# Kernel optimization log

Measured on AMD Instinct MI355X. Metric: run time of the kernel, lower is better.

The kernel has to match this reference:

```python
import jax, jax.numpy as jnp
import numpy as np

DIAG_MASK = 1e20  # value added on the diagonal to exclude self as negative


def setup_inputs() -> dict:
    key = jax.random.key(0)
    k1, k2, k3 = jax.random.split(key, 3)
    B, D_in, D_out = 4096, 1024, 1024
    anchor_x = jax.random.normal(k1, (B, D_in), dtype=jnp.float32)
    pos_x = jax.random.normal(k2, (B, D_in), dtype=jnp.float32)
    W = jax.random.normal(k3, (D_in, D_out), dtype=jnp.float32) * (1.0 / np.sqrt(D_in))
    b = jnp.zeros((D_out,), dtype=jnp.float32)
    return {"anchor_x": anchor_x, "pos_x": pos_x, "W": W, "b": b}


def reference(anchor_x, pos_x, W, b):
    # Encoder: simple dense projection (stand-in for the wrapped BERT encoder).
    anchor = anchor_x @ W + b          # [B, D]
    pos = pos_x @ W + b                # [B, D]

    # Pairwise squared distances dist[i,j] = ||anchor_i - pos_j||^2,
    # computed via the GEMM identity |a|^2 + |p|^2 - 2 a.p (same math as the
    # original broadcasted (a_i - p_j)^2 reduce_sum, far less memory traffic).
    a2 = jnp.sum(anchor * anchor, axis=-1, keepdims=True)       # [B, 1]
    p2 = jnp.sum(pos * pos, axis=-1, keepdims=True).T           # [1, B]
    dist = a2 + p2 - 2.0 * (anchor @ pos.T)                     # [B, B]

    B = dist.shape[0]
    mask_dist = dist + jnp.eye(B, dtype=dist.dtype) * DIAG_MASK  # mask diagonal
    indices = jnp.argmin(mask_dist, axis=-1)                     # [B] hard negatives
    neg = pos[indices]                                           # gather [B, D]

    return jnp.concatenate([anchor, pos, neg], axis=-1)          # [B, 3D]
```

## Files before the change

### kernel.cpp

```cpp
#include <hip/hip_runtime.h>


typedef short s8v __attribute__((ext_vector_type(8)));
typedef float f4v __attribute__((ext_vector_type(4)));
typedef unsigned short u16;

#define B  4096
#define D  1024
#define OLD 3072
#define OLD16 6144
#define LDK 68

__device__ __forceinline__ u16 f2bf(float f) {
  union { float f; unsigned u; } v; v.f = f;
  unsigned r = v.u + 0x7FFFu + ((v.u >> 16) & 1u);
  return (u16)(r >> 16);
}
__device__ __forceinline__ float bf2f(u16 s) {
  union { unsigned u; float f; } v; v.u = ((unsigned)s) << 16;
  return v.f;
}

__device__ __forceinline__ void gld16(const void* g, void* l) {
  __builtin_amdgcn_global_load_lds(
      (const __attribute__((address_space(1))) unsigned int*)g,
      (__attribute__((address_space(3))) unsigned int*)l, 16, 0, 0);
}

struct Top2 { float v1, v2; int j1, j2; };
__device__ __forceinline__ void t2_insert(Top2& t, float v, int j) {
  if (v < t.v1 || (v == t.v1 && j < t.j1)) {
    t.v2 = t.v1; t.j2 = t.j1; t.v1 = v; t.j1 = j;
  } else if (v < t.v2 || (v == t.v2 && j < t.j2)) {
    t.v2 = v; t.j2 = j;
  }
}
struct Top4 { float v[4]; int j[4]; };
__device__ __forceinline__ void t4_insert(Top4& t, float v, int j) {
  if (v < t.v[3] || (v == t.v[3] && j < t.j[3])) {
    int p = 3;
#pragma unroll
    for (int s = 0; s < 3; ++s) {
      if (p > 0 && (v < t.v[p - 1] || (v == t.v[p - 1] && j < t.j[p - 1]))) {
        t.v[p] = t.v[p - 1]; t.j[p] = t.j[p - 1]; --p;
      }
    }
    t.v[p] = v; t.j[p] = j;
  }
}

__global__ void splitT_W(const float* __restrict__ W, u16* __restrict__ WtQ) {
  __shared__ float tile[32][33];
  const int bx = blockIdx.x * 32, by = blockIdx.y * 32;
  const int tx = threadIdx.x, ty = threadIdx.y;
  for (int dy = 0; dy < 32; dy += 8)
    tile[ty + dy][tx] = W[(size_t)(by + ty + dy) * D + bx + tx];
  __syncthreads();
  for (int dy = 0; dy < 32; dy += 8) {
    const float v = tile[tx][ty + dy];
    const u16 h = f2bf(v);
    const size_t o = (size_t)(bx + ty + dy) * 2048 + by + tx;
    WtQ[o] = h;
    WtQ[o + 1024] = f2bf(v - bf2f(h));
  }
}

__global__ __launch_bounds__(256) void splitX2(
    const float* __restrict__ A, const float* __restrict__ P,
    u16* __restrict__ O16, u16* __restrict__ posXq) {
  const int r = blockIdx.x, t = threadIdx.x;
  const bool isPos = r >= B;
  const int row = isPos ? r - B : r;
  const float4 v = *(const float4*)&(isPos ? P : A)[(size_t)row * D + t * 4];
  const float vv[4] = {v.x, v.y, v.z, v.w};
  ushort4 hi, mi;
  u16* hp = &hi.x; u16* mp = &mi.x;
#pragma unroll
  for (int i = 0; i < 4; ++i) {
    hp[i] = f2bf(vv[i]);
    mp[i] = f2bf(vv[i] - bf2f(hp[i]));
  }
  if (isPos) {
    *(ushort4*)&posXq[(size_t)row * 2048 + t * 4] = hi;
    *(ushort4*)&posXq[(size_t)row * 2048 + 1024 + t * 4] = mi;
  } else {
    *(ushort4*)&O16[(size_t)row * OLD16 + 4096 + t * 4] = hi;
    *(ushort4*)&O16[(size_t)row * OLD16 + 5120 + t * 4] = mi;
  }
}

__global__ __launch_bounds__(256) void enc_mfma(
    float* out, const u16* __restrict__ posXq, const u16* __restrict__ WtQ,
    const float* __restrict__ bias, u16* __restrict__ Aq, u16* __restrict__ Pq) {
  __shared__ __align__(16) u16 lAh[128 * 32], lAm[128 * 32];
  __shared__ __align__(16) u16 lBh[128 * 32], lBm[128 * 32];
  const u16* O16 = (const u16*)out;
  const int tid = threadIdx.x, lane = tid & 63, wave = tid >> 6;
  const int waveM = wave >> 1, waveN = wave & 1;
  const int row16 = lane & 15, quad = lane >> 4;
  const bool isPos = blockIdx.y >= 32;
  const int Mbase = (blockIdx.y & 31) * 128;
  const int Nbase = blockIdx.x * 128;
  f4v acc[4][4] = {};

  for (int kk = 0; kk < D; kk += 32) {
    __syncthreads();
#pragma unroll
    for (int i = 0; i < 2; ++i) {
      const int c = i * 256 + wave * 64 + lane;
      const int row = c >> 2, col8 = (c & 3) * 8;
      const int lo = (i * 256 + wave * 64) * 8;
      if (isPos) {
        gld16(&posXq[(size_t)(Mbase + row) * 2048 + kk + col8], &lAh[lo]);
        gld16(&posXq[(size_t)(Mbase + row) * 2048 + 1024 + kk + col8], &lAm[lo]);
      } else {
        gld16(&O16[(size_t)(Mbase + row) * OLD16 + 4096 + kk + col8], &lAh[lo]);
        gld16(&O16[(size_t)(Mbase + row) * OLD16 + 5120 + kk + col8], &lAm[lo]);
      }
      gld16(&WtQ[(size_t)(Nbase + row) * 2048 + kk + col8], &lBh[lo]);
      gld16(&WtQ[(size_t)(Nbase + row) * 2048 + 1024 + kk + col8], &lBm[lo]);
    }
    __syncthreads();
    s8v ah[4], am[4], bh[4], bm[4];
#pragma unroll
    for (int mi = 0; mi < 4; ++mi) {
      const int ro = (waveM * 64 + mi * 16 + row16) * 32 + quad * 8;
      ah[mi] = *(const s8v*)&lAh[ro];
      am[mi] = *(const s8v*)&lAm[ro];
    }
#pragma unroll
    for (int ni = 0; ni < 4; ++ni) {
      const int ro = (waveN * 64 + ni * 16 + row16) * 32 + quad * 8;
      bh[ni] = *(const s8v*)&lBh[ro];
      bm[ni] = *(const s8v*)&lBm[ro];
    }
#pragma unroll
    for (int mi = 0; mi < 4; ++mi)
#pragma unroll
      for (int ni = 0; ni < 4; ++ni) {
        f4v a = acc[mi][ni];
        a = __builtin_amdgcn_mfma_f32_16x16x32_bf16(ah[mi], bh[ni], a, 0, 0, 0);
        a = __builtin_amdgcn_mfma_f32_16x16x32_bf16(ah[mi], bm[ni], a, 0, 0, 0);
        a = __builtin_amdgcn_mfma_f32_16x16x32_bf16(am[mi], bh[ni], a, 0, 0, 0);
        acc[mi][ni] = a;
      }
  }
  const int outOff = isPos ? 1024 : 0;
  u16* Q = isPos ? Pq : Aq;
#pragma unroll
  for (int ni = 0; ni < 4; ++ni) {
    const int col = Nbase + waveN * 64 + ni * 16 + row16;
    const float bv = bias[col];
#pragma unroll
    for (int mi = 0; mi < 4; ++mi) {
      const int rbase = Mbase + waveM * 64 + mi * 16 + quad * 4;
#pragma unroll
      for (int r = 0; r < 4; ++r) {
        const size_t row = rbase + r;
        const float v = acc[mi][ni][r] + bv;
        out[row * OLD + outOff + col] = v;
        const u16 h = f2bf(v);
        Q[row * 2048 + col] = h;
        Q[row * 2048 + 1024 + col] = f2bf(v - bf2f(h));
      }
    }
  }
}

__global__ __launch_bounds__(256) void pnorm(float* __restrict__ o) {
  const int row = blockIdx.x, t = threadIdx.x;
  const float4 v = *(const float4*)&o[(size_t)row * OLD + D + t * 4];
  float s = v.x * v.x + v.y * v.y + v.z * v.z + v.w * v.w;
#pragma unroll
  for (int off = 32; off; off >>= 1) s += __shfl_down(s, off, 64);
  __shared__ float wsum[4];
  if ((t & 63) == 0) wsum[t >> 6] = s;
  __syncthreads();
  if (t == 0) o[(size_t)row * OLD + 2048] = wsum[0] + wsum[1] + wsum[2] + wsum[3];
}

__global__ __launch_bounds__(256) void dist_mfma(
    const u16* __restrict__ Aq, const u16* __restrict__ Pq, float* __restrict__ o) {
  __shared__ __align__(16) u16 lAh[128 * 32], lAm[128 * 32];
  __shared__ __align__(16) u16 lBh[128 * 32];
  __shared__ float sv1[128][2], sv2[128][2];
  __shared__ int sj1[128][2], sj2[128][2];
  const int tid = threadIdx.x, lane = tid & 63, wave = tid >> 6;
  const int waveM = wave >> 1, waveN = wave & 1;
  const int row16 = lane & 15, quad = lane >> 4;
  const int Mbase = blockIdx.y * 128;
  const int Nbase = blockIdx.x * 128;
  f4v acc[4][4] = {};

  for (int kk = 0; kk < D; kk += 32) {
    __syncthreads();
#pragma unroll
    for (int i = 0; i < 2; ++i) {
      const int c = i * 256 + wave * 64 + lane;
      const int row = c >> 2, col8 = (c & 3) * 8;
      const int lo = (i * 256 + wave * 64) * 8;
      gld16(&Aq[(size_t)(Mbase + row) * 2048 + kk + col8], &lAh[lo]);
      gld16(&Aq[(size_t)(Mbase + row) * 2048 + 1024 + kk + col8], &lAm[lo]);
      gld16(&Pq[(size_t)(Nbase + row) * 2048 + kk + col8], &lBh[lo]);
    }
    __syncthreads();
    s8v ah[4], am[4], bh[4];
#pragma unroll
    for (int i = 0; i < 4; ++i) {
      const int aro = (waveM * 64 + i * 16 + row16) * 32 + quad * 8;
      const int bro = (waveN * 64 + i * 16 + row16) * 32 + quad * 8;
      ah[i] = *(const s8v*)&lAh[aro];
      am[i] = *(const s8v*)&lAm[aro];
      bh[i] = *(const s8v*)&lBh[bro];
    }
#pragma unroll
    for (int mi = 0; mi < 4; ++mi)
#pragma unroll
      for (int ni = 0; ni < 4; ++ni) {
        f4v a = acc[mi][ni];
        a = __builtin_amdgcn_mfma_f32_16x16x32_bf16(ah[mi], bh[ni], a, 0, 0, 0);
        a = __builtin_amdgcn_mfma_f32_16x16x32_bf16(am[mi], bh[ni], a, 0, 0, 0);
        acc[mi][ni] = a;
      }
  }

  float p2c[4];
#pragma unroll
  for (int ni = 0; ni < 4; ++ni)
    p2c[ni] = o[(size_t)(Nbase + waveN * 64 + ni * 16 + row16) * OLD + 2048];
#pragma unroll
  for (int mi = 0; mi < 4; ++mi)
#pragma unroll
    for (int r = 0; r < 4; ++r) {
      const int rg = Mbase + waveM * 64 + mi * 16 + quad * 4 + r;
      Top2 tp; tp.v1 = 3.0e38f; tp.v2 = 3.0e38f; tp.j1 = 0; tp.j2 = 1;
#pragma unroll
      for (int ni = 0; ni < 4; ++ni) {
        const int cg = Nbase + waveN * 64 + ni * 16 + row16;
        if (cg != rg) t2_insert(tp, p2c[ni] - 2.0f * acc[mi][ni][r], cg);
      }
#pragma unroll
      for (int m = 1; m < 16; m <<= 1) {
        const float ov1 = __shfl_xor(tp.v1, m, 64);
        const int oj1 = __shfl_xor(tp.j1, m, 64);
        const float ov2 = __shfl_xor(tp.v2, m, 64);
        const int oj2 = __shfl_xor(tp.j2, m, 64);
        t2_insert(tp, ov1, oj1);
        t2_insert(tp, ov2, oj2);
      }
      if (row16 == 0) {
        const int rl = waveM * 64 + mi * 16 + quad * 4 + r;
        sv1[rl][waveN] = tp.v1; sj1[rl][waveN] = tp.j1;
        sv2[rl][waveN] = tp.v2; sj2[rl][waveN] = tp.j2;
      }
    }
  __syncthreads();
  if (tid < 128) {
    Top2 tp; tp.v1 = sv1[tid][0]; tp.j1 = sj1[tid][0];
    tp.v2 = sv2[tid][0]; tp.j2 = sj2[tid][0];
    t2_insert(tp, sv1[tid][1], sj1[tid][1]);
    t2_insert(tp, sv2[tid][1], sj2[tid][1]);
    ((float4*)&o[(size_t)(Mbase + tid) * OLD + 2056])[blockIdx.x] =
        make_float4(tp.v1, __int_as_float(tp.j1), tp.v2, __int_as_float(tp.j2));
  }
}

__global__ __launch_bounds__(256) void argmin_refine(float* __restrict__ o) {
  const int i = blockIdx.x, t = threadIdx.x;
  __shared__ int gj[4];
  if (t < 64) {
    Top4 tp;
#pragma unroll
    for (int c = 0; c < 4; ++c) { tp.v[c] = 3.0e38f; tp.j[c] = 0; }
    if (t < 32) {
      const float4 p = ((const float4*)&o[(size_t)i * OLD + 2056])[t];
      t4_insert(tp, p.x, __float_as_int(p.y));
      t4_insert(tp, p.z, __float_as_int(p.w));
    }
#pragma unroll
    for (int m = 1; m < 32; m <<= 1) {
#pragma unroll
      for (int c = 0; c < 4; ++c) {
        const float ov = __shfl_xor(tp.v[c], m, 64);
        const int oj = __shfl_xor(tp.j[c], m, 64);
        t4_insert(tp, ov, oj);
      }
    }
    if (t == 0) {
#pragma unroll
      for (int c = 0; c < 4; ++c)
        gj[c] = (tp.j[c] < 0) ? 0 : (tp.j[c] > B - 1 ? B - 1 : tp.j[c]);
    }
  }
  __syncthreads();
  int jj[4];
#pragma unroll
  for (int c = 0; c < 4; ++c) jj[c] = gj[c];
  const float4 a4 = *(const float4*)&o[(size_t)i * OLD + t * 4];
  float s[4], n[4];
#pragma unroll
  for (int c = 0; c < 4; ++c) {
    const float4 q = *(const float4*)&o[(size_t)jj[c] * OLD + D + t * 4];
    s[c] = a4.x * q.x + a4.y * q.y + a4.z * q.z + a4.w * q.w;
    n[c] = q.x * q.x + q.y * q.y + q.z * q.z + q.w * q.w;
  }
#pragma unroll
  for (int off = 32; off; off >>= 1)
#pragma unroll
    for (int c = 0; c < 4; ++c) {
      s[c] += __shfl_down(s[c], off, 64);
      n[c] += __shfl_down(n[c], off, 64);
    }
  __shared__ float wsum[4][8];
  __shared__ int sjf;
  if ((t & 63) == 0)
#pragma unroll
    for (int c = 0; c < 4; ++c) {
      wsum[t >> 6][c] = s[c];
      wsum[t >> 6][4 + c] = n[c];
    }
  __syncthreads();
  if (t == 0) {
    float bd = 3.4e38f; int bj = 0x7fffffff;
#pragma unroll
    for (int c = 0; c < 4; ++c) {
      const float S = wsum[0][c] + wsum[1][c] + wsum[2][c] + wsum[3][c];
      const float N = wsum[0][4 + c] + wsum[1][4 + c] + wsum[2][4 + c] + wsum[3][4 + c];
      const float d = N - 2.0f * S;
      const int j = jj[c];
      if (d < bd || (d == bd && j < bj)) { bd = d; bj = j; }
    }
    sjf = bj;
  }
  __syncthreads();
  const int j = sjf;
  ((float4*)&o[(size_t)i * OLD + 2048])[t] = ((const float4*)&o[(size_t)j * OLD + D])[t];
}

__global__ __launch_bounds__(256) void enc_gemm(
    const float* __restrict__ X, const float* __restrict__ W,
    const float* __restrict__ bia, float* __restrict__ out, int outOff) {
  __shared__ float lA[32][LDK];
  __shared__ float lW[32][LDK];
  const int tid = threadIdx.x;
  const int Mbase = blockIdx.y * 64;
  const int Nbase = blockIdx.x * 64;
  const int ty = tid >> 4, tx = tid & 15;
  float acc[4][4] = {};
  for (int k0 = 0; k0 < D; k0 += 32) {
    __syncthreads();
#pragma unroll
    for (int h = 0; h < 2; ++h) {
      const int ch = tid + h * 256;
      const int r = ch >> 3, c4 = (ch & 7) * 4;
      const float4 a4 = *(const float4*)&X[(size_t)(Mbase + r) * D + k0 + c4];
      lA[c4 + 0][r] = a4.x; lA[c4 + 1][r] = a4.y;
      lA[c4 + 2][r] = a4.z; lA[c4 + 3][r] = a4.w;
      const int kr = ch >> 4, nc = (ch & 15) * 4;
      *(float4*)&lW[kr][nc] = *(const float4*)&W[(size_t)(k0 + kr) * D + Nbase + nc];
    }
    __syncthreads();
#pragma unroll
    for (int kk = 0; kk < 32; ++kk) {
      const float4 av = *(const float4*)&lA[kk][ty * 4];
      const float4 wv = *(const float4*)&lW[kk][tx * 4];
      acc[0][0] += av.x * wv.x; acc[0][1] += av.x * wv.y; acc[0][2] += av.x * wv.z; acc[0][3] += av.x * wv.w;
      acc[1][0] += av.y * wv.x; acc[1][1] += av.y * wv.y; acc[1][2] += av.y * wv.z; acc[1][3] += av.y * wv.w;
      acc[2][0] += av.z * wv.x; acc[2][1] += av.z * wv.y; acc[2][2] += av.z * wv.z; acc[2][3] += av.z * wv.w;
      acc[3][0] += av.w * wv.x; acc[3][1] += av.w * wv.y; acc[3][2] += av.w * wv.z; acc[3][3] += av.w * wv.w;
    }
  }
  const float4 b4 = *(const float4*)&bia[Nbase + tx * 4];
#pragma unroll
  for (int i = 0; i < 4; ++i) {
    const int row = Mbase + ty * 4 + i;
    float4 ov;
    ov.x = acc[i][0] + b4.x; ov.y = acc[i][1] + b4.y;
    ov.z = acc[i][2] + b4.z; ov.w = acc[i][3] + b4.w;
    *(float4*)&out[(size_t)row * OLD + outOff + Nbase + tx * 4] = ov;
  }
}

__global__ __launch_bounds__(256) void dist_argmin_f32(float* __restrict__ o) {
  __shared__ float lA[32][LDK];
  __shared__ float lB[32][LDK];
  const int tid = threadIdx.x;
  const int Mbase = blockIdx.y * 64, Nbase = blockIdx.x * 64;
  const int ty = tid >> 4, tx = tid & 15;
  float acc[4][4] = {};
  for (int k0 = 0; k0 < D; k0 += 32) {
    __syncthreads();
#pragma unroll
    for (int h = 0; h < 2; ++h) {
      const int ch = tid + h * 256;
      const int r = ch >> 3, c4 = (ch & 7) * 4;
      const float4 a4 = *(const float4*)&o[(size_t)(Mbase + r) * OLD + k0 + c4];
      const float4 b4 = *(const float4*)&o[(size_t)(Nbase + r) * OLD + D + k0 + c4];
      lA[c4 + 0][r] = a4.x; lA[c4 + 1][r] = a4.y;
      lA[c4 + 2][r] = a4.z; lA[c4 + 3][r] = a4.w;
      lB[c4 + 0][r] = b4.x; lB[c4 + 1][r] = b4.y;
      lB[c4 + 2][r] = b4.z; lB[c4 + 3][r] = b4.w;
    }
    __syncthreads();
#pragma unroll
    for (int kk = 0; kk < 32; ++kk) {
      const float4 av = *(const float4*)&lA[kk][ty * 4];
      const float4 bv = *(const float4*)&lB[kk][tx * 4];
      acc[0][0] += av.x * bv.x; acc[0][1] += av.x * bv.y; acc[0][2] += av.x * bv.z; acc[0][3] += av.x * bv.w;
      acc[1][0] += av.y * bv.x; acc[1][1] += av.y * bv.y; acc[1][2] += av.y * bv.z; acc[1][3] += av.y * bv.w;
      acc[2][0] += av.z * bv.x; acc[2][1] += av.z * bv.y; acc[2][2] += av.z * bv.z; acc[2][3] += av.z * bv.w;
      acc[3][0] += av.w * bv.x; acc[3][1] += av.w * bv.y; acc[3][2] += av.w * bv.z; acc[3][3] += av.w * bv.w;
    }
  }
  float colp2[4];
#pragma unroll
  for (int j = 0; j < 4; ++j)
    colp2[j] = o[(size_t)(Nbase + tx * 4 + j) * OLD + 2048];
#pragma unroll
  for (int i = 0; i < 4; ++i) {
    const int rg = Mbase + ty * 4 + i;
    float bv = 3.0e38f; int bj = 0;
#pragma unroll
    for (int j = 0; j < 4; ++j) {
      const int cg = Nbase + tx * 4 + j;
      const float d = colp2[j] - 2.0f * acc[i][j];
      if (cg != rg && d < bv) { bv = d; bj = cg; }
    }
#pragma unroll
    for (int m = 1; m < 16; m <<= 1) {
      const float ov = __shfl_xor(bv, m, 64);
      const int oj = __shfl_xor(bj, m, 64);
      if (ov < bv || (ov == bv && oj < bj)) { bv = ov; bj = oj; }
    }
    if (tx == 0)
      ((float2*)&o[(size_t)rg * OLD + 2056])[blockIdx.x] =
          make_float2(bv, __int_as_float(bj));
  }
}

__global__ __launch_bounds__(256) void argmin_final_f2(float* __restrict__ o, int nblk) {
  const int i = blockIdx.x, t = threadIdx.x;
  __shared__ int sj;
  if (t < 64) {
    float v = 3.4e38f; int j = 0x7fffffff;
    if (t < nblk) {
      const float2 p = ((const float2*)&o[(size_t)i * OLD + 2056])[t];
      v = p.x; j = __float_as_int(p.y);
    }
#pragma unroll
    for (int m = 32; m; m >>= 1) {
      const float ov = __shfl_xor(v, m, 64);
      const int oj = __shfl_xor(j, m, 64);
      if (ov < v || (ov == v && oj < j)) { v = ov; j = oj; }
    }
    if (t == 0) sj = (j < 0) ? 0 : (j > B - 1 ? B - 1 : j);
  }
  __syncthreads();
  const int j = sj;
  ((float4*)&o[(size_t)i * OLD + 2048])[t] = ((const float4*)&o[(size_t)j * OLD + D])[t];
}

extern "C" void kernel_launch(void* const* d_in, const int* in_sizes, int n_in,
                              void* d_out, int out_size, void* d_ws, size_t ws_size,
                              hipStream_t stream) {
  const float* anchor_x = (const float*)d_in[0];
  const float* pos_x    = (const float*)d_in[1];
  const float* W        = (const float*)d_in[2];
  const float* b        = (const float*)d_in[3];
  float* out = (float*)d_out;
  char* ws = (char*)d_ws;
  const size_t MB = 1024 * 1024;

  if (ws_size >= 52 * MB) {
    u16* Aq     = (u16*)(ws);
    u16* Pq     = (u16*)(ws + 16 * MB);
    u16* WtQ    = (u16*)(ws + 32 * MB);
    u16* posXq  = (u16*)(ws + 36 * MB);
    splitT_W<<<dim3(32, 32), dim3(32, 8), 0, stream>>>(W, WtQ);
    splitX2<<<2 * B, 256, 0, stream>>>(anchor_x, pos_x, (u16*)out, posXq);
    enc_mfma<<<dim3(8, 64), 256, 0, stream>>>(out, posXq, WtQ, b, Aq, Pq);
    pnorm<<<B, 256, 0, stream>>>(out);
    dist_mfma<<<dim3(32, 32), 256, 0, stream>>>(Aq, Pq, out);
    argmin_refine<<<B, 256, 0, stream>>>(out);
  } else {
    enc_gemm<<<dim3(16, 64), 256, 0, stream>>>(anchor_x, W, b, out, 0);
    enc_gemm<<<dim3(16, 64), 256, 0, stream>>>(pos_x,    W, b, out, 1024);
    pnorm<<<B, 256, 0, stream>>>(out);
    dist_argmin_f32<<<dim3(64, 64), 256, 0, stream>>>(out);
    argmin_final_f2<<<B, 256, 0, stream>>>(out, 64);
  }
}
```

Measured before the change: 318.6 us.

## Use single fp16 MFMA for distance GEMM with double-buffered swizzled LDS

The distance GEMM now stores anchor and positive embeddings as one fp16 value each instead of a bf16 hi/lo pair. This halves that GEMM's operand traffic and MFMA count, since two bf16 MFMAs per tile become one fp16 MFMA. Both the encoder and distance GEMMs also gain double-buffered LDS staging with an XOR swizzle on the K-chunk slot, so the next tile loads while the current one computes and LDS bank conflicts are reduced. The cost is lower precision in the dot products that feed the coarse argmin, which a later refine pass must absorb, and the doubled LDS footprint may lower occupancy.

```diff
diff --git a/kernel.cpp b/kernel.cpp
--- a/kernel.cpp
+++ b/kernel.cpp
@@ -2,6 +2,7 @@
 
 
 typedef short s8v __attribute__((ext_vector_type(8)));
+typedef _Float16 h8v __attribute__((ext_vector_type(8)));
 typedef float f4v __attribute__((ext_vector_type(4)));
 typedef unsigned short u16;
 
@@ -91,9 +92,10 @@
 
 __global__ __launch_bounds__(256) void enc_mfma(
     float* out, const u16* __restrict__ posXq, const u16* __restrict__ WtQ,
-    const float* __restrict__ bias, u16* __restrict__ Aq, u16* __restrict__ Pq) {
-  __shared__ __align__(16) u16 lAh[128 * 32], lAm[128 * 32];
-  __shared__ __align__(16) u16 lBh[128 * 32], lBm[128 * 32];
+    const float* __restrict__ bias, _Float16* __restrict__ Aq,
+    _Float16* __restrict__ Pq) {
+  __shared__ __align__(16) u16 lAh[2][128 * 32], lAm[2][128 * 32];
+  __shared__ __align__(16) u16 lBh[2][128 * 32], lBm[2][128 * 32];
   const u16* O16 = (const u16*)out;
   const int tid = threadIdx.x, lane = tid & 63, wave = tid >> 6;
   const int waveM = wave >> 1, waveN = wave & 1;
@@ -103,36 +105,46 @@
   const int Nbase = blockIdx.x * 128;
   f4v acc[4][4] = {};
 
-  for (int kk = 0; kk < D; kk += 32) {
-    __syncthreads();
+  auto STAGE = [&](int buf, int kk) {
 #pragma unroll
     for (int i = 0; i < 2; ++i) {
-      const int c = i * 256 + wave * 64 + lane;
-      const int row = c >> 2, col8 = (c & 3) * 8;
-      const int lo = (i * 256 + wave * 64) * 8;
+      const int c = i * 256 + tid;
+      const int row = c >> 2;
+      const int col8 = ((c & 3) ^ ((row >> 1) & 3)) * 8;
+      u16* ah = &lAh[buf][(i * 256 + wave * 64) * 8];
+      u16* am = &lAm[buf][(i * 256 + wave * 64) * 8];
+      u16* bh = &lBh[buf][(i * 256 + wave * 64) * 8];
+      u16* bm = &lBm[buf][(i * 256 + wave * 64) * 8];
       if (isPos) {
-        gld16(&posXq[(size_t)(Mbase + row) * 2048 + kk + col8], &lAh[lo]);
-        gld16(&posXq[(size_t)(Mbase + row) * 2048 + 1024 + kk + col8], &lAm[lo]);
+        gld16(&posXq[(size_t)(Mbase + row) * 2048 + kk + col8], ah);
+        gld16(&posXq[(size_t)(Mbase + row) * 2048 + 1024 + kk + col8], am);
       } else {
-        gld16(&O16[(size_t)(Mbase + row) * OLD16 + 4096 + kk + col8], &lAh[lo]);
-        gld16(&O16[(size_t)(Mbase + row) * OLD16 + 5120 + kk + col8], &lAm[lo]);
-      }
-      gld16(&WtQ[(size_t)(Nbase + row) * 2048 + kk + col8], &lBh[lo]);
-      gld16(&WtQ[(size_t)(Nbase + row) * 2048 + 1024 + kk + col8], &lBm[lo]);
-    }
-    __syncthreads();
+        gld16(&O16[(size_t)(Mbase + row) * OLD16 + 4096 + kk + col8], ah);
+        gld16(&O16[(size_t)(Mbase + row) * OLD16 + 5120 + kk + col8], am);
+      }
+      gld16(&WtQ[(size_t)(Nbase + row) * 2048 + kk + col8], bh);
+      gld16(&WtQ[(size_t)(Nbase + row) * 2048 + 1024 + kk + col8], bm);
+    }
+  };
+
+  STAGE(0, 0);
+  __syncthreads();
+  int cur = 0;
+  const int slot = (quad ^ ((row16 >> 1) & 3)) * 8;
+  for (int t = 1; t <= 32; ++t) {
+    if (t < 32) STAGE(cur ^ 1, t * 32);
     s8v ah[4], am[4], bh[4], bm[4];
 #pragma unroll
     for (int mi = 0; mi < 4; ++mi) {
-      const int ro = (waveM * 64 + mi * 16 + row16) * 32 + quad * 8;
-      ah[mi] = *(const s8v*)&lAh[ro];
-      am[mi] = *(const s8v*)&lAm[ro];
+      const int ro = (waveM * 64 + mi * 16 + row16) * 32 + slot;
+      ah[mi] = *(const s8v*)&lAh[cur][ro];
+      am[mi] = *(const s8v*)&lAm[cur][ro];
     }
 #pragma unroll
     for (int ni = 0; ni < 4; ++ni) {
-      const int ro = (waveN * 64 + ni * 16 + row16) * 32 + quad * 8;
-      bh[ni] = *(const s8v*)&lBh[ro];
-      bm[ni] = *(const s8v*)&lBm[ro];
+      const int ro = (waveN * 64 + ni * 16 + row16) * 32 + slot;
+      bh[ni] = *(const s8v*)&lBh[cur][ro];
+      bm[ni] = *(const s8v*)&lBm[cur][ro];
     }
 #pragma unroll
     for (int mi = 0; mi < 4; ++mi)
@@ -144,9 +156,11 @@
         a = __builtin_amdgcn_mfma_f32_16x16x32_bf16(am[mi], bh[ni], a, 0, 0, 0);
         acc[mi][ni] = a;
       }
+    __syncthreads();
+    cur ^= 1;
   }
   const int outOff = isPos ? 1024 : 0;
-  u16* Q = isPos ? Pq : Aq;
+  _Float16* Q = isPos ? Pq : Aq;
 #pragma unroll
   for (int ni = 0; ni < 4; ++ni) {
     const int col = Nbase + waveN * 64 + ni * 16 + row16;
@@ -159,9 +173,7 @@
         const size_t row = rbase + r;
         const float v = acc[mi][ni][r] + bv;
         out[row * OLD + outOff + col] = v;
-        const u16 h = f2bf(v);
-        Q[row * 2048 + col] = h;
-        Q[row * 2048 + 1024 + col] = f2bf(v - bf2f(h));
+        Q[row * 1024 + col] = (_Float16)v;
       }
     }
   }
@@ -180,9 +192,10 @@
 }
 
 __global__ __launch_bounds__(256) void dist_mfma(
-    const u16* __restrict__ Aq, const u16* __restrict__ Pq, float* __restrict__ o) {
-  __shared__ __align__(16) u16 lAh[128 * 32], lAm[128 * 32];
-  __shared__ __align__(16) u16 lBh[128 * 32];
+    const _Float16* __restrict__ Aq, const _Float16* __restrict__ Pq,
+    float* __restrict__ o) {
+  __shared__ __align__(16) u16 lA[2][128 * 32];
+  __shared__ __align__(16) u16 lB[2][128 * 32];
   __shared__ float sv1[128][2], sv2[128][2];
   __shared__ int sj1[128][2], sj2[128][2];
   const int tid = threadIdx.x, lane = tid & 63, wave = tid >> 6;
@@ -192,36 +205,39 @@
   const int Nbase = blockIdx.x * 128;
   f4v acc[4][4] = {};
 
-  for (int kk = 0; kk < D; kk += 32) {
+  auto STAGE = [&](int buf, int kk) {
+#pragma unroll
+    for (int i = 0; i < 2; ++i) {
+      const int c = i * 256 + tid;
+      const int row = c >> 2;
+      const int col8 = ((c & 3) ^ ((row >> 1) & 3)) * 8;
+      u16* la = &lA[buf][(i * 256 + wave * 64) * 8];
+      u16* lb = &lB[buf][(i * 256 + wave * 64) * 8];
+      gld16(&Aq[(size_t)(Mbase + row) * 1024 + kk + col8], la);
+      gld16(&Pq[(size_t)(Nbase + row) * 1024 + kk + col8], lb);
+    }
+  };
+
+  STAGE(0, 0);
+  __syncthreads();
+  int cur = 0;
+  const int slot = (quad ^ ((row16 >> 1) & 3)) * 8;
+  for (int t = 1; t <= 32; ++t) {
+    if (t < 32) STAGE(cur ^ 1, t * 32);
+    h8v a[4], b[4];
+#pragma unroll
+    for (int i = 0; i < 4; ++i) {
+      a[i] = *(const h8v*)&lA[cur][(waveM * 64 + i * 16 + row16) * 32 + slot];
+      b[i] = *(const h8v*)&lB[cur][(waveN * 64 + i * 16 + row16) * 32 + slot];
+    }
+#pragma unroll
+    for (int mi = 0; mi < 4; ++mi)
+#pragma unroll
+      for (int ni = 0; ni < 4; ++ni)
+        acc[mi][ni] =
+            __builtin_amdgcn_mfma_f32_16x16x32_f16(a[mi], b[ni], acc[mi][ni], 0, 0, 0);
     __syncthreads();
-#pragma unroll
-    for (int i = 0; i < 2; ++i) {
-      const int c = i * 256 + wave * 64 + lane;
-      const int row = c >> 2, col8 = (c & 3) * 8;
-      const int lo = (i * 256 + wave * 64) * 8;
-      gld16(&Aq[(size_t)(Mbase + row) * 2048 + kk + col8], &lAh[lo]);
-      gld16(&Aq[(size_t)(Mbase + row) * 2048 + 1024 + kk + col8], &lAm[lo]);
-      gld16(&Pq[(size_t)(Nbase + row) * 2048 + kk + col8], &lBh[lo]);
-    }
-    __syncthreads();
-    s8v ah[4], am[4], bh[4];
-#pragma unroll
-    for (int i = 0; i < 4; ++i) {
-      const int aro = (waveM * 64 + i * 16 + row16) * 32 + quad * 8;
-      const int bro = (waveN * 64 + i * 16 + row16) * 32 + quad * 8;
-      ah[i] = *(const s8v*)&lAh[aro];
-      am[i] = *(const s8v*)&lAm[aro];
-      bh[i] = *(const s8v*)&lBh[bro];
-    }
-#pragma unroll
-    for (int mi = 0; mi < 4; ++mi)
-#pragma unroll
-      for (int ni = 0; ni < 4; ++ni) {
-        f4v a = acc[mi][ni];
-        a = __builtin_amdgcn_mfma_f32_16x16x32_bf16(ah[mi], bh[ni], a, 0, 0, 0);
-        a = __builtin_amdgcn_mfma_f32_16x16x32_bf16(am[mi], bh[ni], a, 0, 0, 0);
-        acc[mi][ni] = a;
-      }
+    cur ^= 1;
   }
 
   float p2c[4];
@@ -471,11 +487,11 @@
   char* ws = (char*)d_ws;
   const size_t MB = 1024 * 1024;
 
-  if (ws_size >= 52 * MB) {
-    u16* Aq     = (u16*)(ws);
-    u16* Pq     = (u16*)(ws + 16 * MB);
-    u16* WtQ    = (u16*)(ws + 32 * MB);
-    u16* posXq  = (u16*)(ws + 36 * MB);
+  if (ws_size >= 36 * MB) {
+    _Float16* Aq = (_Float16*)(ws);
+    _Float16* Pq = (_Float16*)(ws + 8 * MB);
+    u16* WtQ     = (u16*)(ws + 16 * MB);
+    u16* posXq   = (u16*)(ws + 20 * MB);
     splitT_W<<<dim3(32, 32), dim3(32, 8), 0, stream>>>(W, WtQ);
     splitX2<<<2 * B, 256, 0, stream>>>(anchor_x, pos_x, (u16*)out, posXq);
     enc_mfma<<<dim3(8, 64), 256, 0, stream>>>(out, posXq, WtQ, b, Aq, Pq);
```

Result: slower. 343.4 us (+7.8%).
